# Performance work log

Measured on AMD Instinct MI355X. Metric: run time of the kernel, lower is better.

Reference implementation:

```python
import jax, jax.numpy as jnp
import numpy as np

N_NODES = 100_000
N_RAND_EDGES = 3_200_000
IN_FEATS, HIDDEN, N_CLASSES = 256, 32, 40


def setup_inputs() -> dict:
    key = jax.random.key(0)
    kf, ks, kd, kw1, kw2 = jax.random.split(key, 5)
    features = jax.random.normal(kf, (N_NODES, IN_FEATS), dtype=jnp.float32)
    # random edges + explicit self loops (mirrors dgl.add_self_loop)
    src = jnp.concatenate([
        jax.random.randint(ks, (N_RAND_EDGES,), 0, N_NODES, dtype=jnp.int32),
        jnp.arange(N_NODES, dtype=jnp.int32),
    ])
    dst = jnp.concatenate([
        jax.random.randint(kd, (N_RAND_EDGES,), 0, N_NODES, dtype=jnp.int32),
        jnp.arange(N_NODES, dtype=jnp.int32),
    ])
    # Glorot-style init as in DGL GraphConv
    W1 = jax.random.normal(kw1, (IN_FEATS, HIDDEN), dtype=jnp.float32) * (2.0 / (IN_FEATS + HIDDEN)) ** 0.5
    b1 = jnp.zeros((HIDDEN,), dtype=jnp.float32)
    W2 = jax.random.normal(kw2, (HIDDEN, N_CLASSES), dtype=jnp.float32) * (2.0 / (HIDDEN + N_CLASSES)) ** 0.5
    b2 = jnp.zeros((N_CLASSES,), dtype=jnp.float32)
    return {"features": features, "src": src, "dst": dst,
            "W1": W1, "b1": b1, "W2": W2, "b2": b2}


def _graph_conv(x, W, b, src, dst, norm_src, norm_dst):
    """DGL GraphConv, norm='both': D_in^{-1/2} A D_out^{-1/2} X W + b.
    Apply W first (cheaper gather when out_feats small); math-identical."""
    h = (x * norm_src[:, None]) @ W              # [N, out]
    msgs = h[src]                                # gather  [E, out]
    agg = jax.ops.segment_sum(msgs, dst, num_segments=N_NODES)  # scatter-add
    return agg * norm_dst[:, None] + b


def reference(features, src, dst, W1, b1, W2, b2):
    ones = jnp.ones(src.shape[0], dtype=jnp.float32)
    out_deg = jax.ops.segment_sum(ones, src, num_segments=N_NODES)
    in_deg = jax.ops.segment_sum(ones, dst, num_segments=N_NODES)
    norm_src = jax.lax.rsqrt(out_deg)            # self loops guarantee deg >= 1
    norm_dst = jax.lax.rsqrt(in_deg)

    x = _graph_conv(features, W1, b1, src, dst, norm_src, norm_dst)
    x = jax.nn.relu(x)
    # F.dropout(training=self.training) is identity at inference
    x = _graph_conv(x, W2, b2, src, dst, norm_src, norm_dst)
    return jax.nn.log_softmax(x, axis=1)
```

## Files before the change

### kernel.cpp

```cpp
#include <hip/hip_runtime.h>
#include <hip/hip_bf16.h>
#include <math.h>

#define BSHIFT 7
#define NBUCK(N) (((N) + 127) >> 7)
#define TILE 8192
#define CAP 5632
#define CAPS 2040
#define NXCD 8

typedef short bf16x8 __attribute__((ext_vector_type(8)));
typedef float f32x16 __attribute__((ext_vector_type(16)));

__device__ __forceinline__ unsigned short f2bf(float f) {
    unsigned u = __float_as_uint(f);
    u += 0x7fffu + ((u >> 16) & 1u);
    return (unsigned short)(u >> 16);
}
__device__ __forceinline__ unsigned packbf2(float lo, float hi) {
    return (unsigned)f2bf(lo) | ((unsigned)f2bf(hi) << 16);
}
__device__ __forceinline__ float bf_lo(unsigned u) { return __uint_as_float(u << 16); }
__device__ __forceinline__ float bf_hi(unsigned u) { return __uint_as_float(u & 0xffff0000u); }

__device__ __forceinline__ int xcc_id() {
    int x;
    asm volatile("s_getreg_b32 %0, hwreg(HW_REG_XCC_ID)" : "=s"(x));
    return x & (NXCD - 1);
}

__global__ __launch_bounds__(256) void pg_kernel(
    const int* __restrict__ src, const int* __restrict__ dst,
    int* __restrict__ gcurD, int* __restrict__ gcurS,
    int* __restrict__ gbufD, unsigned char* __restrict__ gbufS,
    const float* __restrict__ feat, const float* __restrict__ W1,
    unsigned short* __restrict__ h1, int E, int K, int PB, int N) {
    __shared__ char smem[16896];
    const int t = threadIdx.x;

    if (blockIdx.x < PB) {
        int* cD = (int*)smem;
        int* bD = cD + 800;
        int* cS = bD + 800;
        int* bS = cS + 800;
        const int tile = blockIdx.x * TILE;
        const int vx = xcc_id();
        for (int i = t; i < K; i += 256) { cD[i] = 0; cS[i] = 0; }
        __syncthreads();

        int dv[32];
        #pragma unroll
        for (int i = 0; i < 32; ++i) {
            const int e = tile + i * 256 + t;
            dv[i] = (e < E) ? dst[e] : -1;
            if (dv[i] >= 0) {
                atomicAdd(&cD[dv[i] >> BSHIFT], 1);
                atomicAdd(&cS[src[e] >> BSHIFT], 1);
            }
        }
        __syncthreads();
        for (int i = t; i < K; i += 256) {
            int c = cD[i];
            bD[i] = (c ? atomicAdd(&gcurD[i], c) : 0) + i * CAP;
            cD[i] = 0;
            c = cS[i];
            bS[i] = (c ? atomicAdd(&gcurS[vx * K + i], c) : 0) + (vx * K + i) * CAPS;
            cS[i] = 0;
        }
        __syncthreads();
        #pragma unroll
        for (int i = 0; i < 32; ++i) {
            if (dv[i] >= 0) {
                const int e = tile + i * 256 + t;
                const int sv = src[e];
                const int b1 = dv[i] >> BSHIFT;
                const int p1 = bD[b1] + atomicAdd(&cD[b1], 1);
                gbufD[p1] = ((dv[i] & 127) << 17) | sv;
                const int b2 = sv >> BSHIFT;
                const int p2 = bS[b2] + atomicAdd(&cS[b2], 1);
                gbufS[p2] = (unsigned char)(sv & 127);
            }
        }
    } else {
        short* W1t = (short*)smem;
        for (int i = t; i < 8192; i += 256) {
            const int k = i >> 5, c = i & 31;
            W1t[c * 264 + k] = (short)f2bf(W1[i]);
        }
        __syncthreads();

        const int l  = t & 63;
        const int wv = t >> 6;
        const int base = (blockIdx.x - PB) * 128 + wv * 32;
        const int m  = l & 31;
        const int kh = (l >> 5) << 3;
        int r = base + m;
        if (r >= N) r = N - 1;
        const float* fr = feat + (size_t)r * 256 + kh;
        const short* wr = &W1t[m * 264 + kh];

        f32x16 acc;
        #pragma unroll
        for (int i = 0; i < 16; ++i) acc[i] = 0.f;

        #pragma unroll
        for (int kb = 0; kb < 16; ++kb) {
            const float4 f0 = *(const float4*)(fr + kb * 16);
            const float4 f1 = *(const float4*)(fr + kb * 16 + 4);
            bf16x8 a;
            a[0] = (short)f2bf(f0.x); a[1] = (short)f2bf(f0.y);
            a[2] = (short)f2bf(f0.z); a[3] = (short)f2bf(f0.w);
            a[4] = (short)f2bf(f1.x); a[5] = (short)f2bf(f1.y);
            a[6] = (short)f2bf(f1.z); a[7] = (short)f2bf(f1.w);
            const bf16x8 b = *(const bf16x8*)(wr + kb * 16);
            acc = __builtin_amdgcn_mfma_f32_32x32x16_bf16(a, b, acc, 0, 0, 0);
        }

        const int rbase = base + ((l >> 5) << 2);
        #pragma unroll
        for (int reg = 0; reg < 16; ++reg) {
            const int row = rbase + (reg & 3) + ((reg >> 2) << 3);
            if (row < N)
                h1[(size_t)row * 32 + m] = f2bf(acc[reg]);
        }
    }
}

__global__ __launch_bounds__(256) void fillS_kernel(
    const int* __restrict__ cntS, const unsigned char* __restrict__ gbufS,
    float* __restrict__ nsrc, unsigned* __restrict__ h1, int N, int K) {
    __shared__ int cnt[128];
    __shared__ float sns[128];
    const int t = threadIdx.x;
    const int b = blockIdx.x;
    if (t < 128) cnt[t] = 0;
    __syncthreads();
    for (int x = 0; x < NXCD; ++x) {
        const int seg = x * K + b;
        const int bs = seg * CAPS;
        const int be = bs + min(cntS[seg], CAPS);
        for (int idx = bs + t; idx < be; idx += 256)
            atomicAdd(&cnt[gbufS[idx]], 1);
    }
    __syncthreads();
    if (t < 128) {
        const float v = rsqrtf((float)cnt[t]);
        sns[t] = v;
        const int n = (b << BSHIFT) + t;
        if (n < N) nsrc[n] = v;
    }
    __syncthreads();
    const int node = t >> 1;
    const int n = (b << BSHIFT) + node;
    if (n < N) {
        const float ns = sns[node];
        unsigned* row = h1 + (size_t)n * 16 + (t & 1) * 8;
        uint4 q0 = *(uint4*)row;
        uint4 q1 = *(uint4*)(row + 4);
        q0.x = packbf2(bf_lo(q0.x) * ns, bf_hi(q0.x) * ns);
        q0.y = packbf2(bf_lo(q0.y) * ns, bf_hi(q0.y) * ns);
        q0.z = packbf2(bf_lo(q0.z) * ns, bf_hi(q0.z) * ns);
        q0.w = packbf2(bf_lo(q0.w) * ns, bf_hi(q0.w) * ns);
        q1.x = packbf2(bf_lo(q1.x) * ns, bf_hi(q1.x) * ns);
        q1.y = packbf2(bf_lo(q1.y) * ns, bf_hi(q1.y) * ns);
        q1.z = packbf2(bf_lo(q1.z) * ns, bf_hi(q1.z) * ns);
        q1.w = packbf2(bf_lo(q1.w) * ns, bf_hi(q1.w) * ns);
        *(uint4*)row = q0;
        *(uint4*)(row + 4) = q1;
    }
}

__global__ __launch_bounds__(512) void fda1_kernel(
    const int* __restrict__ cntD, int* __restrict__ gbufD,
    const unsigned* __restrict__ h1, const float* __restrict__ nsrc,
    const float* __restrict__ b1, int* __restrict__ rowstart,
    int* __restrict__ indeg, float* __restrict__ ndst,
    unsigned* __restrict__ x1s, int N, int K) {
    __shared__ int lraw[CAP];
    __shared__ int lcsr[CAP];
    __shared__ int cnt[128], sc[128], cur[128];
    __shared__ float sb1[32];
    const int t = threadIdx.x;
    const int b = blockIdx.x;
    if (t < 128) cnt[t] = 0;
    if (t >= 128 && t < 160) sb1[t - 128] = b1[t - 128];
    __syncthreads();

    const int bs = b * CAP;
    const int total = min(cntD[b], CAP);
    for (int i = t; i < total; i += 512) {
        const int v = gbufD[bs + i];
        lraw[i] = v;
        atomicAdd(&cnt[v >> 17], 1);
    }
    __syncthreads();
    if (t < 128) sc[t] = cnt[t];
    __syncthreads();
    for (int off = 1; off < 128; off <<= 1) {
        int x = (t < 128 && t >= off) ? sc[t - off] : 0;
        __syncthreads();
        if (t < 128) sc[t] += x;
        __syncthreads();
    }
    if (t < 128) {
        const int deg = cnt[t];
        cur[t] = sc[t] - deg;
        const int n = (b << BSHIFT) + t;
        if (n < N) {
            rowstart[n] = bs + sc[t] - deg;
            indeg[n] = deg;
            ndst[n] = rsqrtf((float)deg);
        }
    }
    __syncthreads();
    for (int i = t; i < total; i += 512) {
        const int v = lraw[i];
        const int pos = atomicAdd(&cur[v >> 17], 1);
        lcsr[pos] = v & 131071;
    }
    __syncthreads();
    for (int i = t; i < total; i += 512) gbufD[bs + i] = lcsr[i];

    const int c  = t & 3;
    const int eg = (t >> 2) & 1;
    const uint4* H = (const uint4*)h1;
    for (int half = 0; half < 2; ++half) {
        const int node = (t >> 3) + half * 64;
        const int n = (b << BSHIFT) + node;
        if (n >= N) continue;
        const int deg = cnt[node];
        const int re = sc[node];
        const int rs = re - deg;
        const int n8 = deg >> 3;
        float a0=0.f,a1=0.f,a2=0.f,a3=0.f,a4=0.f,a5=0.f,a6=0.f,a7=0.f;
        float d0=0.f,d1=0.f,d2=0.f,d3=0.f,d4=0.f,d5=0.f,d6=0.f,d7=0.f;
        for (int i = 0; i < n8; ++i) {
            const int k0 = rs + i * 8 + eg * 4;
            const int s0 = lcsr[k0],     s1 = lcsr[k0 + 1];
            const int s2 = lcsr[k0 + 2], s3 = lcsr[k0 + 3];
            const uint4 q0 = H[(size_t)s0 * 4 + c];
            const uint4 q1 = H[(size_t)s1 * 4 + c];
            const uint4 q2 = H[(size_t)s2 * 4 + c];
            const uint4 q3 = H[(size_t)s3 * 4 + c];
            a0 += bf_lo(q0.x); a1 += bf_hi(q0.x);
            a2 += bf_lo(q0.y); a3 += bf_hi(q0.y);
            a4 += bf_lo(q0.z); a5 += bf_hi(q0.z);
            a6 += bf_lo(q0.w); a7 += bf_hi(q0.w);
            d0 += bf_lo(q1.x); d1 += bf_hi(q1.x);
            d2 += bf_lo(q1.y); d3 += bf_hi(q1.y);
            d4 += bf_lo(q1.z); d5 += bf_hi(q1.z);
            d6 += bf_lo(q1.w); d7 += bf_hi(q1.w);
            a0 += bf_lo(q2.x); a1 += bf_hi(q2.x);
            a2 += bf_lo(q2.y); a3 += bf_hi(q2.y);
            a4 += bf_lo(q2.z); a5 += bf_hi(q2.z);
            a6 += bf_lo(q2.w); a7 += bf_hi(q2.w);
            d0 += bf_lo(q3.x); d1 += bf_hi(q3.x);
            d2 += bf_lo(q3.y); d3 += bf_hi(q3.y);
            d4 += bf_lo(q3.z); d5 += bf_hi(q3.z);
            d6 += bf_lo(q3.w); d7 += bf_hi(q3.w);
        }
        for (int k = rs + n8 * 8 + eg; k < re; k += 2) {
            const int s0 = lcsr[k];
            const uint4 q0 = H[(size_t)s0 * 4 + c];
            a0 += bf_lo(q0.x); a1 += bf_hi(q0.x);
            a2 += bf_lo(q0.y); a3 += bf_hi(q0.y);
            a4 += bf_lo(q0.z); a5 += bf_hi(q0.z);
            a6 += bf_lo(q0.w); a7 += bf_hi(q0.w);
        }
        a0 += d0; a1 += d1; a2 += d2; a3 += d3;
        a4 += d4; a5 += d5; a6 += d6; a7 += d7;
        a0 += __shfl_xor(a0, 4, 64); a1 += __shfl_xor(a1, 4, 64);
        a2 += __shfl_xor(a2, 4, 64); a3 += __shfl_xor(a3, 4, 64);
        a4 += __shfl_xor(a4, 4, 64); a5 += __shfl_xor(a5, 4, 64);
        a6 += __shfl_xor(a6, 4, 64); a7 += __shfl_xor(a7, 4, 64);
        if (eg == 0) {
            const float nd = rsqrtf((float)deg);
            const float ns = nsrc[n];
            const float* bb = sb1 + c * 8;
            float x0 = fmaxf(a0 * nd + bb[0], 0.f) * ns;
            float x1 = fmaxf(a1 * nd + bb[1], 0.f) * ns;
            float x2 = fmaxf(a2 * nd + bb[2], 0.f) * ns;
            float x3 = fmaxf(a3 * nd + bb[3], 0.f) * ns;
            float x4 = fmaxf(a4 * nd + bb[4], 0.f) * ns;
            float x5 = fmaxf(a5 * nd + bb[5], 0.f) * ns;
            float x6 = fmaxf(a6 * nd + bb[6], 0.f) * ns;
            float x7 = fmaxf(a7 * nd + bb[7], 0.f) * ns;
            uint4 o;
            o.x = packbf2(x0, x1); o.y = packbf2(x2, x3);
            o.z = packbf2(x4, x5); o.w = packbf2(x6, x7);
            ((uint4*)x1s)[(size_t)n * 4 + c] = o;
        }
    }
}

__global__ __launch_bounds__(256) void agg2f_kernel(
    const int* __restrict__ csr_src, const int* __restrict__ rowstart,
    const int* __restrict__ indeg, const unsigned* __restrict__ x1s,
    const float* __restrict__ ndst, const float* __restrict__ W2,
    const float* __restrict__ b2, float* __restrict__ out, int N) {
    __shared__ float sW2[32 * 40];
    __shared__ float sb2[40];
    const int t = threadIdx.x;
    for (int i = t; i < 1280; i += 256) sW2[i] = W2[i];
    if (t < 40) sb2[t] = b2[t];
    __syncthreads();
    const int n = blockIdx.x * 32 + (t >> 3);
    if (n >= N) return;
    const int c  = t & 3;
    const int eg = (t >> 2) & 1;
    const int rs = rowstart[n];
    const int deg = indeg[n];
    const int re = rs + deg;
    const int n8 = deg >> 3;
    float a0=0.f,a1=0.f,a2=0.f,a3=0.f,a4=0.f,a5=0.f,a6=0.f,a7=0.f;
    float d0=0.f,d1=0.f,d2=0.f,d3=0.f,d4=0.f,d5=0.f,d6=0.f,d7=0.f;
    const uint4* H = (const uint4*)x1s;
    for (int i = 0; i < n8; ++i) {
        const int k0 = rs + i * 8 + eg * 4;
        const int s0 = csr_src[k0],     s1 = csr_src[k0 + 1];
        const int s2 = csr_src[k0 + 2], s3 = csr_src[k0 + 3];
        const uint4 q0 = H[(size_t)s0 * 4 + c];
        const uint4 q1 = H[(size_t)s1 * 4 + c];
        const uint4 q2 = H[(size_t)s2 * 4 + c];
        const uint4 q3 = H[(size_t)s3 * 4 + c];
        a0 += bf_lo(q0.x); a1 += bf_hi(q0.x);
        a2 += bf_lo(q0.y); a3 += bf_hi(q0.y);
        a4 += bf_lo(q0.z); a5 += bf_hi(q0.z);
        a6 += bf_lo(q0.w); a7 += bf_hi(q0.w);
        d0 += bf_lo(q1.x); d1 += bf_hi(q1.x);
        d2 += bf_lo(q1.y); d3 += bf_hi(q1.y);
        d4 += bf_lo(q1.z); d5 += bf_hi(q1.z);
        d6 += bf_lo(q1.w); d7 += bf_hi(q1.w);
        a0 += bf_lo(q2.x); a1 += bf_hi(q2.x);
        a2 += bf_lo(q2.y); a3 += bf_hi(q2.y);
        a4 += bf_lo(q2.z); a5 += bf_hi(q2.z);
        a6 += bf_lo(q2.w); a7 += bf_hi(q2.w);
        d0 += bf_lo(q3.x); d1 += bf_hi(q3.x);
        d2 += bf_lo(q3.y); d3 += bf_hi(q3.y);
        d4 += bf_lo(q3.z); d5 += bf_hi(q3.z);
        d6 += bf_lo(q3.w); d7 += bf_hi(q3.w);
    }
    for (int k = rs + n8 * 8 + eg; k < re; k += 2) {
        const int s0 = csr_src[k];
        const uint4 q0 = H[(size_t)s0 * 4 + c];
        a0 += bf_lo(q0.x); a1 += bf_hi(q0.x);
        a2 += bf_lo(q0.y); a3 += bf_hi(q0.y);
        a4 += bf_lo(q0.z); a5 += bf_hi(q0.z);
        a6 += bf_lo(q0.w); a7 += bf_hi(q0.w);
    }
    a0 += d0; a1 += d1; a2 += d2; a3 += d3;
    a4 += d4; a5 += d5; a6 += d6; a7 += d7;
    a0 += __shfl_xor(a0, 4, 64); a1 += __shfl_xor(a1, 4, 64);
    a2 += __shfl_xor(a2, 4, 64); a3 += __shfl_xor(a3, 4, 64);
    a4 += __shfl_xor(a4, 4, 64); a5 += __shfl_xor(a5, 4, 64);
    a6 += __shfl_xor(a6, 4, 64); a7 += __shfl_xor(a7, 4, 64);
    const float nd = ndst[n];
    const float v0 = a0 * nd, v1 = a1 * nd, v2 = a2 * nd, v3 = a3 * nd;
    const float v4 = a4 * nd, v5 = a5 * nd, v6 = a6 * nd, v7 = a7 * nd;

    const int j = t & 7;
    float z[5];
    #pragma unroll
    for (int u = 0; u < 5; ++u) z[u] = sb2[j * 5 + u];
    const int gbase = (t & 63) & ~7;
    #pragma unroll
    for (int cc = 0; cc < 4; ++cc) {
        const int sl = gbase + cc;
        const float w0 = __shfl(v0, sl, 64);
        const float w1 = __shfl(v1, sl, 64);
        const float w2 = __shfl(v2, sl, 64);
        const float w3 = __shfl(v3, sl, 64);
        const float w4 = __shfl(v4, sl, 64);
        const float w5 = __shfl(v5, sl, 64);
        const float w6 = __shfl(v6, sl, 64);
        const float w7 = __shfl(v7, sl, 64);
        const float* Wr = &sW2[(cc * 8) * 40 + j * 5];
        #pragma unroll
        for (int u = 0; u < 5; ++u) {
            z[u] += w0 * Wr[u]       + w1 * Wr[40 + u]  + w2 * Wr[80 + u]  + w3 * Wr[120 + u]
                  + w4 * Wr[160 + u] + w5 * Wr[200 + u] + w6 * Wr[240 + u] + w7 * Wr[280 + u];
        }
    }
    float m = z[0];
    #pragma unroll
    for (int u = 1; u < 5; ++u) m = fmaxf(m, z[u]);
    m = fmaxf(m, __shfl_xor(m, 1, 64));
    m = fmaxf(m, __shfl_xor(m, 2, 64));
    m = fmaxf(m, __shfl_xor(m, 4, 64));
    float s = 0.f;
    #pragma unroll
    for (int u = 0; u < 5; ++u) s += __expf(z[u] - m);
    s += __shfl_xor(s, 1, 64);
    s += __shfl_xor(s, 2, 64);
    s += __shfl_xor(s, 4, 64);
    const float ls = __logf(s);
    float* op = out + (size_t)n * 40 + j * 5;
    #pragma unroll
    for (int u = 0; u < 5; ++u) op[u] = z[u] - m - ls;
}

extern "C" void kernel_launch(void* const* d_in, const int* in_sizes, int n_in,
                              void* d_out, int out_size, void* d_ws, size_t ws_size,
                              hipStream_t stream) {
    const float* feat = (const float*)d_in[0];
    const int*   src  = (const int*)d_in[1];
    const int*   dst  = (const int*)d_in[2];
    const float* W1   = (const float*)d_in[3];
    const float* b1   = (const float*)d_in[4];
    const float* W2   = (const float*)d_in[5];
    const float* b2   = (const float*)d_in[6];
    float* out = (float*)d_out;

    const int N = in_sizes[0] / 256;
    const int E = in_sizes[1];
    const int K = NBUCK(N);

    char* p = (char*)d_ws;
    float* nsrc = (float*)p;                 p += (size_t)N * 4;
    float* ndst = (float*)p;                 p += (size_t)N * 4;
    unsigned* h1  = (unsigned*)p;            p += (size_t)N * 64;
    unsigned* x1s = (unsigned*)p;            p += (size_t)N * 64;
    char* a2dead = (char*)p;                 p += (size_t)N * 128;
    int* rowstart = (int*)p;                 p += (size_t)N * 4;
    int* indeg_i  = (int*)p;                 p += (size_t)N * 4;
    int* gcurD    = (int*)p;                 p += 800 * 4;
    int* gcurS    = (int*)p;                 p += (size_t)NXCD * 800 * 4;
    int* gbufD    = (int*)p;                 p += (size_t)K * CAP * 4;
    unsigned char* gbufS = (unsigned char*)a2dead;

    hipMemsetAsync(gcurD, 0, sizeof(int) * (800 + NXCD * 800), stream);

    const int PB = (E + TILE - 1) / TILE;
    const int GB = (N + 127) / 128;

    pg_kernel<<<PB + GB, 256, 0, stream>>>(src, dst, gcurD, gcurS, gbufD, gbufS,
                                           feat, W1, (unsigned short*)h1, E, K, PB, N);
    fillS_kernel<<<K, 256, 0, stream>>>(gcurS, gbufS, nsrc, h1, N, K);
    fda1_kernel<<<K, 512, 0, stream>>>(gcurD, gbufD, h1, nsrc, b1,
                                       rowstart, indeg_i, ndst, x1s, N, K);
    agg2f_kernel<<<(N + 31) / 32, 256, 0, stream>>>(gbufD, rowstart, indeg_i, x1s, ndst, W2, b2, out, N);
}
```

Measured before the change: 342.4 us.

## Split dst-bucket counters per XCD and shrink partition tiles

Gives the dst-bucket atomic cursors one slice per XCD, each with its own sub-capacity region, so global atomics for a bucket stay within one XCD's L2 instead of contending across dies. The fda1 kernel now gathers the eight per-XCD sub-buckets into its local arrays before the CSR sort. The partition tile shrinks from 8192 to 2048 edges, which gives more partition blocks and fewer registers per thread. The trade-offs are more global atomics from more blocks and a fixed per-XCD capacity of 704 entries, which could overflow if edges land unevenly across XCDs.

```diff
diff --git a/kernel.cpp b/kernel.cpp
--- a/kernel.cpp
+++ b/kernel.cpp
@@ -4,8 +4,9 @@
 
 #define BSHIFT 7
 #define NBUCK(N) (((N) + 127) >> 7)
-#define TILE 8192
+#define TILE 2048
 #define CAP 5632
+#define CAPXD 704
 #define CAPS 2040
 #define NXCD 8
 
@@ -48,9 +49,9 @@
         for (int i = t; i < K; i += 256) { cD[i] = 0; cS[i] = 0; }
         __syncthreads();
 
-        int dv[32];
-        #pragma unroll
-        for (int i = 0; i < 32; ++i) {
+        int dv[8];
+        #pragma unroll
+        for (int i = 0; i < 8; ++i) {
             const int e = tile + i * 256 + t;
             dv[i] = (e < E) ? dst[e] : -1;
             if (dv[i] >= 0) {
@@ -61,7 +62,7 @@
         __syncthreads();
         for (int i = t; i < K; i += 256) {
             int c = cD[i];
-            bD[i] = (c ? atomicAdd(&gcurD[i], c) : 0) + i * CAP;
+            bD[i] = (c ? atomicAdd(&gcurD[i * NXCD + vx], c) : 0) + (i * NXCD + vx) * CAPXD;
             cD[i] = 0;
             c = cS[i];
             bS[i] = (c ? atomicAdd(&gcurS[vx * K + i], c) : 0) + (vx * K + i) * CAPS;
@@ -69,7 +70,7 @@
         }
         __syncthreads();
         #pragma unroll
-        for (int i = 0; i < 32; ++i) {
+        for (int i = 0; i < 8; ++i) {
             if (dv[i] >= 0) {
                 const int e = tile + i * 256 + t;
                 const int sv = src[e];
@@ -179,19 +180,31 @@
     __shared__ int lraw[CAP];
     __shared__ int lcsr[CAP];
     __shared__ int cnt[128], sc[128], cur[128];
+    __shared__ int scnt[NXCD];
     __shared__ float sb1[32];
     const int t = threadIdx.x;
     const int b = blockIdx.x;
     if (t < 128) cnt[t] = 0;
+    if (t < NXCD) scnt[t] = min(cntD[b * NXCD + t], CAPXD);
     if (t >= 128 && t < 160) sb1[t - 128] = b1[t - 128];
     __syncthreads();
 
-    const int bs = b * CAP;
-    const int total = min(cntD[b], CAP);
-    for (int i = t; i < total; i += 512) {
-        const int v = gbufD[bs + i];
-        lraw[i] = v;
-        atomicAdd(&cnt[v >> 17], 1);
+    int soff[NXCD];
+    {
+        int acc = 0;
+        #pragma unroll
+        for (int x = 0; x < NXCD; ++x) { soff[x] = acc; acc += scnt[x]; }
+    }
+    const int total = soff[NXCD - 1] + scnt[NXCD - 1];
+
+    for (int x = 0; x < NXCD; ++x) {
+        const int bs = (b * NXCD + x) * CAPXD;
+        const int c0 = scnt[x], o0 = soff[x];
+        for (int i = t; i < c0; i += 512) {
+            const int v = gbufD[bs + i];
+            lraw[o0 + i] = v;
+            atomicAdd(&cnt[v >> 17], 1);
+        }
     }
     __syncthreads();
     if (t < 128) sc[t] = cnt[t];
@@ -207,7 +220,7 @@
         cur[t] = sc[t] - deg;
         const int n = (b << BSHIFT) + t;
         if (n < N) {
-            rowstart[n] = bs + sc[t] - deg;
+            rowstart[n] = b * CAP + sc[t] - deg;
             indeg[n] = deg;
             ndst[n] = rsqrtf((float)deg);
         }
@@ -219,7 +232,7 @@
         lcsr[pos] = v & 131071;
     }
     __syncthreads();
-    for (int i = t; i < total; i += 512) gbufD[bs + i] = lcsr[i];
+    for (int i = t; i < total; i += 512) gbufD[b * CAP + i] = lcsr[i];
 
     const int c  = t & 3;
     const int eg = (t >> 2) & 1;
@@ -423,12 +436,12 @@
     char* a2dead = (char*)p;                 p += (size_t)N * 128;
     int* rowstart = (int*)p;                 p += (size_t)N * 4;
     int* indeg_i  = (int*)p;                 p += (size_t)N * 4;
-    int* gcurD    = (int*)p;                 p += 800 * 4;
+    int* gcurD    = (int*)p;                 p += (size_t)800 * NXCD * 4;
     int* gcurS    = (int*)p;                 p += (size_t)NXCD * 800 * 4;
     int* gbufD    = (int*)p;                 p += (size_t)K * CAP * 4;
     unsigned char* gbufS = (unsigned char*)a2dead;
 
-    hipMemsetAsync(gcurD, 0, sizeof(int) * (800 + NXCD * 800), stream);
+    hipMemsetAsync(gcurD, 0, sizeof(int) * (size_t)800 * NXCD * 2, stream);
 
     const int PB = (E + TILE - 1) / TILE;
     const int GB = (N + 127) / 128;
```

After: 382.2 us. 11.6% more time.
